# Performance work log

Measured on AMD Instinct MI355X. Metric: run time of the kernel, lower is better.

Reference implementation:

```python
import jax, jax.numpy as jnp
import numpy as np
from jax import lax

SEQ, BATCH, IN, HID = 4096, 8, 1024, 1024


def setup_inputs() -> dict:
    key = jax.random.key(0)
    k1, k2 = jax.random.split(key)
    X = jax.random.normal(k1, (SEQ, BATCH, IN), dtype=jnp.float32)
    hidden = jnp.zeros((BATCH, HID), dtype=jnp.float32)  # None init == zeros
    W = jax.random.normal(k2, (3 * HID, IN), dtype=jnp.float32) * 0.02
    b = jnp.zeros((3 * HID,), dtype=jnp.float32)
    return {"X": X, "hidden": hidden, "W": W, "b": b}


def reference(X, hidden, W, b):
    # window=1: source = X; Y = Linear(X) -> [S, B, 3H]
    Y = jnp.einsum('sbi,hi->sbh', X, W) + b
    Z, F, O = jnp.split(Y, 3, axis=2)
    Z = jnp.tanh(Z)
    F = jax.nn.sigmoid(F)

    # ForgetMult: c_t = f_t * z_t + (1 - f_t) * c_{t-1}
    def step(c, fz):
        f, z = fz
        c = f * z + (1.0 - f) * c
        return c, c

    _, C = lax.scan(step, hidden, (F, Z))  # C: [S, B, H]
    H = jax.nn.sigmoid(O) * C
    return (H, C[-1:, :, :], C)
```

## Files before the change

### kernel.cpp

```cpp
#include <hip/hip_runtime.h>
#include <hip/hip_bf16.h>
#include <stdint.h>

#define S_   4096
#define B_   8
#define IN_  1024
#define H_   1024
#define M_   (S_ * B_)
#define N_   (3 * H_)
#define K_   IN_
#define CH_  (B_ * H_)
#define NC_  64
#define T_   (S_ / NC_)

typedef unsigned short u16;
typedef __bf16 bf16x8 __attribute__((ext_vector_type(8)));
typedef float  f32x4  __attribute__((ext_vector_type(4)));

__device__ __forceinline__ u16 f2bf(float f) {
  unsigned u = __float_as_uint(f);
  u += 0x7fffu + ((u >> 16) & 1u);
  return (u16)(u >> 16);
}

__device__ __forceinline__ float sigmoid_(float x) { return 1.0f / (1.0f + __expf(-x)); }
__device__ __forceinline__ float tanh_(float x)    { return 2.0f / (1.0f + __expf(-2.0f * x)) - 1.0f; }

__global__ void cvt_bf16_kernel(const float* __restrict__ in, u16* __restrict__ out, int n8) {
  int i = blockIdx.x * blockDim.x + threadIdx.x;
  if (i >= n8) return;
  const float4* p = (const float4*)in;
  float4 a = p[2 * i], b = p[2 * i + 1];
  alignas(16) u16 us[8] = {f2bf(a.x), f2bf(a.y), f2bf(a.z), f2bf(a.w),
                           f2bf(b.x), f2bf(b.y), f2bf(b.z), f2bf(b.w)};
  ((uint4*)out)[i] = *(const uint4*)us;
}

#define SWZ(x) ((x) ^ (((x) >> 3) & 0x30))

#define DS_A(s, h, mh) do {                                                    \
  const char* base_ = (const char*)As_[(s)*2+(h)];                             \
  af[0] = *(const bf16x8*)(base_ + aoff[mh][0]);                               \
  af[1] = *(const bf16x8*)(base_ + aoff[mh][1]);                               \
  af[2] = *(const bf16x8*)(base_ + aoff[mh][2]);                               \
  af[3] = *(const bf16x8*)(base_ + aoff[mh][3]);                               \
} while (0)

#define DS_B(s, h) do {                                                        \
  const char* base_ = (const char*)Bs_[(s)*2+(h)];                             \
  bfr[0] = *(const bf16x8*)(base_ + boff[0]);                                  \
  bfr[1] = *(const bf16x8*)(base_ + boff[1]);                                  \
  bfr[2] = *(const bf16x8*)(base_ + boff[2]);                                  \
  bfr[3] = *(const bf16x8*)(base_ + boff[3]);                                  \
} while (0)

#define MMA(mh) do {                                                           \
  __builtin_amdgcn_s_setprio(1);                                              \
  _Pragma("unroll")                                                            \
  for (int fi_ = 0; fi_ < 4; ++fi_)                                            \
    _Pragma("unroll")                                                          \
    for (int fj_ = 0; fj_ < 4; ++fj_)                                          \
      acc[(mh)*4+fi_][fj_] = __builtin_amdgcn_mfma_f32_16x16x32_bf16(          \
          af[fi_], bfr[fj_], acc[(mh)*4+fi_][fj_], 0, 0, 0);                   \
  __builtin_amdgcn_s_setprio(0);                                              \
} while (0)

#define PH_SYNC() do {                                                         \
  asm volatile("" ::: "memory");                                               \
  __builtin_amdgcn_s_barrier();                                                \
  asm volatile("s_waitcnt lgkmcnt(0)" ::: "memory");                           \
} while (0)

#define PH_END() do {                                                          \
  asm volatile("" ::: "memory");                                               \
  __builtin_amdgcn_s_barrier();                                                \
} while (0)

#define VW(n) asm volatile("s_waitcnt vmcnt(" #n ")" ::: "memory")

__global__ __launch_bounds__(512, 2) void gemm_act(
    const u16* __restrict__ Ab, const u16* __restrict__ Bb,
    const float* __restrict__ bias,
    float* __restrict__ zt,
    float* __restrict__ Cf,
    float* __restrict__ Ho) {
  __shared__ alignas(16) u16 As_[4][8192];
  __shared__ alignas(16) u16 Bs_[4][8192];

  const int tid = threadIdx.x;
  const int w = tid >> 6, l = tid & 63;
  const int m0 = blockIdx.y * 256, n0 = blockIdx.x * 256;
  const int wmo = (w >> 2) * 128, wno = (w & 3) * 64;
  const int lr = l & 15, lq = l >> 4;

  const int D0b  = w * 1024 + l * 16;
  const int row0 = D0b >> 6;
  const int c0   = (SWZ(D0b) & 63) >> 1;

  int aoff[2][4], boff[4];
#pragma unroll
  for (int mh = 0; mh < 2; ++mh)
#pragma unroll
    for (int fi = 0; fi < 4; ++fi)
      aoff[mh][fi] = SWZ((wmo + (mh * 4 + fi) * 16 + lr) * 64 + lq * 16);
#pragma unroll
  for (int fj = 0; fj < 4; ++fj)
    boff[fj] = SWZ((wno + fj * 16 + lr) * 64 + lq * 16);

  auto stage = [&](const u16* __restrict__ G, int rb, int tt, int hh, u16* dstp) {
    const u16* s0 = G + (size_t)(rb + row0) * K_ + (tt * 64 + hh * 32 + c0);
    __builtin_amdgcn_global_load_lds(
        (const __attribute__((address_space(1))) void*)s0,
        (__attribute__((address_space(3))) void*)(dstp + (D0b >> 1)), 16, 0, 0);
    const u16* s1 = s0 + (size_t)128 * K_;
    __builtin_amdgcn_global_load_lds(
        (const __attribute__((address_space(1))) void*)s1,
        (__attribute__((address_space(3))) void*)(dstp + (D0b >> 1) + 4096), 16, 0, 0);
  };

  f32x4 acc[8][4] = {};
  bf16x8 af[4], bfr[4];

  stage(Ab, m0, 0, 0, As_[0]); stage(Bb, n0, 0, 0, Bs_[0]);
  stage(Ab, m0, 0, 1, As_[1]); stage(Bb, n0, 0, 1, Bs_[1]);
  stage(Ab, m0, 1, 0, As_[2]); stage(Bb, n0, 1, 0, Bs_[2]);
  VW(4);
  PH_END();

  for (int i = 0; i < 7; ++i) {
    const int t1 = 2 * i + 1, t2 = 2 * i + 2, t3 = 2 * i + 3;
    DS_A(0, 0, 0); DS_B(0, 0); stage(Ab, m0, t1, 1, As_[3]);
    PH_SYNC(); MMA(0); PH_END();
    DS_A(0, 0, 1);             stage(Bb, n0, t1, 1, Bs_[3]);
    PH_SYNC(); MMA(1); PH_END();
    DS_A(0, 1, 0); DS_B(0, 1); stage(Ab, m0, t2, 0, As_[0]);
    PH_SYNC(); MMA(0); PH_END();
    DS_A(0, 1, 1);             stage(Bb, n0, t2, 0, Bs_[0]); VW(4);
    PH_SYNC(); MMA(1); PH_END();
    DS_A(1, 0, 0); DS_B(1, 0); stage(Ab, m0, t2, 1, As_[1]);
    PH_SYNC(); MMA(0); PH_END();
    DS_A(1, 0, 1);             stage(Bb, n0, t2, 1, Bs_[1]);
    PH_SYNC(); MMA(1); PH_END();
    DS_A(1, 1, 0); DS_B(1, 1); stage(Ab, m0, t3, 0, As_[2]);
    PH_SYNC(); MMA(0); PH_END();
    DS_A(1, 1, 1);             stage(Bb, n0, t3, 0, Bs_[2]); VW(4);
    PH_SYNC(); MMA(1); PH_END();
  }

  DS_A(0, 0, 0); DS_B(0, 0); stage(Ab, m0, 15, 1, As_[3]);
  PH_SYNC(); MMA(0); PH_END();
  DS_A(0, 0, 1);             stage(Bb, n0, 15, 1, Bs_[3]);
  PH_SYNC(); MMA(1); PH_END();
  DS_A(0, 1, 0); DS_B(0, 1);
  PH_SYNC(); MMA(0); PH_END();
  DS_A(0, 1, 1); VW(0);
  PH_SYNC(); MMA(1); PH_END();
  DS_A(1, 0, 0); DS_B(1, 0);
  PH_SYNC(); MMA(0); PH_END();
  DS_A(1, 0, 1);
  PH_SYNC(); MMA(1); PH_END();
  DS_A(1, 1, 0); DS_B(1, 1);
  PH_SYNC(); MMA(0); PH_END();
  DS_A(1, 1, 1);
  PH_SYNC(); MMA(1); PH_END();

  const int seg = n0 >> 10;
  const int nh0 = (n0 & 1023) + wno;
  float* dst = (seg == 0) ? zt : (seg == 1 ? Cf : Ho);
#pragma unroll
  for (int fj = 0; fj < 4; ++fj) {
    const int nn = nh0 + fj * 16 + lr;
    const float bv = bias[seg * 1024 + nn];
#pragma unroll
    for (int fi = 0; fi < 8; ++fi) {
#pragma unroll
      for (int rr = 0; rr < 4; ++rr) {
        const int mm = m0 + wmo + fi * 16 + lq * 4 + rr;
        const float v = acc[fi][fj][rr] + bv;
        dst[(size_t)mm * H_ + nn] = (seg == 0) ? tanh_(v) : sigmoid_(v);
      }
    }
  }
}

__global__ void scanA(const float* __restrict__ Cf, const float* __restrict__ zt,
                      float* __restrict__ ckA, float* __restrict__ ckC) {
  const int ch2 = blockIdx.x * 256 + threadIdx.x;
  const int j   = blockIdx.y;
  size_t base2 = (size_t)j * T_ * (CH_ / 2) + ch2;
  const float2* Cf2 = (const float2*)Cf;
  const float2* zt2 = (const float2*)zt;
  float2 A = {1.f, 1.f}, c = {0.f, 0.f};
  for (int tt = 0; tt < T_; ++tt) {
    const float2 f = Cf2[base2];
    const float2 z = zt2[base2];
    const float omx = 1.f - f.x, omy = 1.f - f.y;
    c.x = f.x * z.x + omx * c.x;
    c.y = f.y * z.y + omy * c.y;
    A.x *= omx;
    A.y *= omy;
    base2 += CH_ / 2;
  }
  ((float2*)ckA)[(size_t)j * (CH_ / 2) + ch2] = A;
  ((float2*)ckC)[(size_t)j * (CH_ / 2) + ch2] = c;
}

__global__ void scanComb(const float* __restrict__ ckA, const float* __restrict__ ckC,
                         const float* __restrict__ hidden, float* __restrict__ carry) {
  const int ch = blockIdx.x * 64 + threadIdx.x;
  float c = hidden[ch];
  for (int j = 0; j < NC_; ++j) {
    carry[j * CH_ + ch] = c;
    c = ckC[j * CH_ + ch] + ckA[j * CH_ + ch] * c;
  }
}

__global__ void scanB(float* __restrict__ Cf,
                      const float* __restrict__ zt,
                      float* __restrict__ Ho,
                      float* __restrict__ Clast,
                      const float* __restrict__ carry) {
  const int ch2 = blockIdx.x * 256 + threadIdx.x;
  const int j   = blockIdx.y;
  size_t base2 = (size_t)j * T_ * (CH_ / 2) + ch2;
  float2* Cf2 = (float2*)Cf;
  const float2* zt2 = (const float2*)zt;
  float2* Ho2 = (float2*)Ho;
  float2 c = ((const float2*)carry)[(size_t)j * (CH_ / 2) + ch2];
  for (int tt = 0; tt < T_; ++tt) {
    const float2 f  = Cf2[base2];
    const float2 z  = zt2[base2];
    const float2 so = Ho2[base2];
    c.x = f.x * z.x + (1.f - f.x) * c.x;
    c.y = f.y * z.y + (1.f - f.y) * c.y;
    Cf2[base2] = c;
    Ho2[base2] = float2{so.x * c.x, so.y * c.y};
    base2 += CH_ / 2;
  }
  if (j == NC_ - 1) ((float2*)Clast)[ch2] = c;
}

extern "C" void kernel_launch(void* const* d_in, const int* in_sizes, int n_in,
                              void* d_out, int out_size, void* d_ws, size_t ws_size,
                              hipStream_t stream) {
  const float* X    = (const float*)d_in[0];
  const float* hid  = (const float*)d_in[1];
  const float* W    = (const float*)d_in[2];
  const float* bias = (const float*)d_in[3];

  float* out   = (float*)d_out;
  float* Ho    = out;
  float* Clast = out + (size_t)M_ * H_;
  float* Cf    = Clast + CH_;

  char* ws = (char*)d_ws;
  u16*  Xb    = (u16*)ws;
  u16*  Wb    = (u16*)(ws + 67108864);
  float* zt   = (float*)(ws + 73400320);
  float* ckA  = (float*)(ws + 207618048);
  float* ckC  = (float*)(ws + 209715200);
  float* carry= (float*)(ws + 211812352);

  cvt_bf16_kernel<<<(M_ * K_ / 8 + 255) / 256, 256, 0, stream>>>(X, Xb, M_ * K_ / 8);
  cvt_bf16_kernel<<<(N_ * K_ / 8 + 255) / 256, 256, 0, stream>>>(W, Wb, N_ * K_ / 8);
  gemm_act<<<dim3(N_ / 256, M_ / 256), 512, 0, stream>>>(Xb, Wb, bias, zt, Cf, Ho);
  scanA<<<dim3(CH_ / 512, NC_), 256, 0, stream>>>(Cf, zt, ckA, ckC);
  scanComb<<<CH_ / 64, 64, 0, stream>>>(ckA, ckC, hid, carry);
  scanB<<<dim3(CH_ / 512, NC_), 256, 0, stream>>>(Cf, zt, Ho, Clast, carry);
}
```

Before: 797.6 us.

## Fuse chunked scan phases into one cooperative kernel and merge bf16 conversions

Replaces the three-kernel chunked scan (local chunk scan, carry combine, final rescan) with a single cooperative kernel that uses a grid-wide sync. After the sync, each block recomputes its incoming carry by folding the prefix chunk summaries itself, so the serial combine kernel is no longer needed. The two fp32-to-bf16 conversion launches are also merged into one. This removes launch overhead and the tiny serial combine, at the cost of a grid barrier and redundant prefix work per block, and it requires all 1024 blocks to be co-resident. If the cooperative launch fails, the code falls back to the original three kernels.

```diff
diff --git a/kernel.cpp b/kernel.cpp
--- a/kernel.cpp
+++ b/kernel.cpp
@@ -1,6 +1,9 @@
 #include <hip/hip_runtime.h>
 #include <hip/hip_bf16.h>
+#include <hip/hip_cooperative_groups.h>
 #include <stdint.h>
+
+namespace cg = cooperative_groups;
 
 #define S_   4096
 #define B_   8
@@ -26,14 +29,19 @@
 __device__ __forceinline__ float sigmoid_(float x) { return 1.0f / (1.0f + __expf(-x)); }
 __device__ __forceinline__ float tanh_(float x)    { return 2.0f / (1.0f + __expf(-2.0f * x)) - 1.0f; }
 
-__global__ void cvt_bf16_kernel(const float* __restrict__ in, u16* __restrict__ out, int n8) {
+__global__ void cvt_all(const float* __restrict__ X, const float* __restrict__ W,
+                        u16* __restrict__ Xb, u16* __restrict__ Wb) {
+  const int nX = M_ * K_ / 8, nW = N_ * K_ / 8;
   int i = blockIdx.x * blockDim.x + threadIdx.x;
-  if (i >= n8) return;
+  const float* in; u16* out; int j;
+  if (i < nX)           { in = X; out = Xb; j = i; }
+  else if (i < nX + nW) { in = W; out = Wb; j = i - nX; }
+  else return;
   const float4* p = (const float4*)in;
-  float4 a = p[2 * i], b = p[2 * i + 1];
+  float4 a = p[2 * j], b = p[2 * j + 1];
   alignas(16) u16 us[8] = {f2bf(a.x), f2bf(a.y), f2bf(a.z), f2bf(a.w),
                            f2bf(b.x), f2bf(b.y), f2bf(b.z), f2bf(b.w)};
-  ((uint4*)out)[i] = *(const uint4*)us;
+  ((uint4*)out)[j] = *(const uint4*)us;
 }
 
 #define SWZ(x) ((x) ^ (((x) >> 3) & 0x30))
@@ -183,6 +191,62 @@
   }
 }
 
+__global__ void fused_scan(float* __restrict__ Cf,
+                           const float* __restrict__ zt,
+                           float* __restrict__ Ho,
+                           float* __restrict__ Clast,
+                           const float* __restrict__ hidden,
+                           float* __restrict__ ckA, float* __restrict__ ckC) {
+  cg::grid_group grid = cg::this_grid();
+  const int ch2 = blockIdx.x * 256 + threadIdx.x;
+  const int j   = blockIdx.y;
+  const float2* Cf2c = (const float2*)Cf;
+  const float2* zt2  = (const float2*)zt;
+
+  size_t base2 = (size_t)j * T_ * (CH_ / 2) + ch2;
+  float2 A = {1.f, 1.f}, c = {0.f, 0.f};
+  for (int tt = 0; tt < T_; ++tt) {
+    const float2 f = Cf2c[base2];
+    const float2 z = zt2[base2];
+    const float omx = 1.f - f.x, omy = 1.f - f.y;
+    c.x = f.x * z.x + omx * c.x;
+    c.y = f.y * z.y + omy * c.y;
+    A.x *= omx;
+    A.y *= omy;
+    base2 += CH_ / 2;
+  }
+  ((float2*)ckA)[(size_t)j * (CH_ / 2) + ch2] = A;
+  ((float2*)ckC)[(size_t)j * (CH_ / 2) + ch2] = c;
+
+  grid.sync();
+
+  float2 cin = ((const float2*)hidden)[ch2];
+  const float2* a2 = (const float2*)ckA;
+  const float2* c2 = (const float2*)ckC;
+  for (int jp = 0; jp < j; ++jp) {
+    const float2 Aj = a2[(size_t)jp * (CH_ / 2) + ch2];
+    const float2 Cj = c2[(size_t)jp * (CH_ / 2) + ch2];
+    cin.x = Cj.x + Aj.x * cin.x;
+    cin.y = Cj.y + Aj.y * cin.y;
+  }
+
+  float2 cc = cin;
+  base2 = (size_t)j * T_ * (CH_ / 2) + ch2;
+  float2* Cf2 = (float2*)Cf;
+  float2* Ho2 = (float2*)Ho;
+  for (int tt = 0; tt < T_; ++tt) {
+    const float2 f  = Cf2[base2];
+    const float2 z  = zt2[base2];
+    const float2 so = Ho2[base2];
+    cc.x = f.x * z.x + (1.f - f.x) * cc.x;
+    cc.y = f.y * z.y + (1.f - f.y) * cc.y;
+    Cf2[base2] = cc;
+    Ho2[base2] = float2{so.x * cc.x, so.y * cc.y};
+    base2 += CH_ / 2;
+  }
+  if (j == NC_ - 1) ((float2*)Clast)[ch2] = cc;
+}
+
 __global__ void scanA(const float* __restrict__ Cf, const float* __restrict__ zt,
                       float* __restrict__ ckA, float* __restrict__ ckC) {
   const int ch2 = blockIdx.x * 256 + threadIdx.x;
@@ -215,10 +279,8 @@
   }
 }
 
-__global__ void scanB(float* __restrict__ Cf,
-                      const float* __restrict__ zt,
-                      float* __restrict__ Ho,
-                      float* __restrict__ Clast,
+__global__ void scanB(float* __restrict__ Cf, const float* __restrict__ zt,
+                      float* __restrict__ Ho, float* __restrict__ Clast,
                       const float* __restrict__ carry) {
   const int ch2 = blockIdx.x * 256 + threadIdx.x;
   const int j   = blockIdx.y;
@@ -261,10 +323,21 @@
   float* ckC  = (float*)(ws + 209715200);
   float* carry= (float*)(ws + 211812352);
 
-  cvt_bf16_kernel<<<(M_ * K_ / 8 + 255) / 256, 256, 0, stream>>>(X, Xb, M_ * K_ / 8);
-  cvt_bf16_kernel<<<(N_ * K_ / 8 + 255) / 256, 256, 0, stream>>>(W, Wb, N_ * K_ / 8);
+  const int nAll = M_ * K_ / 8 + N_ * K_ / 8;
+  cvt_all<<<(nAll + 255) / 256, 256, 0, stream>>>(X, W, Xb, Wb);
   gemm_act<<<dim3(N_ / 256, M_ / 256), 512, 0, stream>>>(Xb, Wb, bias, zt, Cf, Ho);
-  scanA<<<dim3(CH_ / 512, NC_), 256, 0, stream>>>(Cf, zt, ckA, ckC);
-  scanComb<<<CH_ / 64, 64, 0, stream>>>(ckA, ckC, hid, carry);
-  scanB<<<dim3(CH_ / 512, NC_), 256, 0, stream>>>(Cf, zt, Ho, Clast, carry);
-}
+
+  {
+    float* CfA = Cf; const float* ztA = zt; float* HoA = Ho; float* ClA = Clast;
+    const float* hiA = hid; float* ckAA = ckA; float* ckCA = ckC;
+    void* args[] = {&CfA, &ztA, &HoA, &ClA, &hiA, &ckAA, &ckCA};
+    hipError_t e = hipLaunchCooperativeKernel((const void*)fused_scan,
+                                              dim3(CH_ / 512, NC_), dim3(256),
+                                              args, 0, stream);
+    if (e != hipSuccess) {
+      scanA<<<dim3(CH_ / 512, NC_), 256, 0, stream>>>(Cf, zt, ckA, ckC);
+      scanComb<<<CH_ / 64, 64, 0, stream>>>(ckA, ckC, hid, carry);
+      scanB<<<dim3(CH_ / 512, NC_), 256, 0, stream>>>(Cf, zt, Ho, Clast, carry);
+    }
+  }
+}
```

Measured after the change: 919.2 us. 15.2% more time.
